# Kernel tuning notes

Measured on AMD Instinct MI355X. Metric: run time of the kernel, lower is better.

Reference implementation:

```python
import jax, jax.numpy as jnp
import numpy as np

K = 3  # kernel_size from init_kwargs


def setup_inputs() -> dict:
    key = jax.random.key(0)
    x = jax.random.normal(key, (32, 64, 56, 56), dtype=jnp.float32)
    return {"x": x}


def reference(x):
    # Faithful translation of Shift.forward: for each channel i, for each
    # (dy, dx) in the kernel window, emit the padded slice
    # x_pad[:, i, dy:dy+h, dx:dx+w]. Concatenation order is channel-major,
    # then row-major over (dy, dx), which equals stacking the k*k shifts on
    # a new axis right after the channel axis and flattening.
    n, c, h, w = x.shape
    pad = K // 2
    xp = jnp.pad(x, ((0, 0), (0, 0), (pad, pad), (pad, pad)))
    # k*k shifted views of shape [n, c, h, w]; loop is over a small fixed
    # offset set (9 for k=3), not over data dims.
    shifts = jnp.stack(
        [xp[:, :, dy:dy + h, dx:dx + w] for dy in range(K) for dx in range(K)],
        axis=2,
    )  # [n, c, k*k, h, w]
    return shifts.reshape(n, c * K * K, h, w)
```

## Files before the change

### kernel.cpp

```cpp
#include <hip/hip_runtime.h>


#define N_ 32
#define C_ 64
#define H_ 56
#define W_ 56
#define KK 9
#define W4 (W_ / 4)
#define ROW_F4 W4
#define OUT_F4 (N_ * C_ * KK * H_ * W4)

__global__ __launch_bounds__(256) void shift_kernel(const float* __restrict__ x,
                                                    float4* __restrict__ out) {
    int idx = blockIdx.x * blockDim.x + threadIdx.x;
    if (idx >= OUT_F4) return;

    int w4 = idx % W4;
    int t  = idx / W4;
    int h  = t % H_;
    t /= H_;
    int s  = t % KK;
    t /= KK;
    int c  = t % C_;
    int n  = t / C_;

    int dy = s / 3 - 1;
    int dx = s % 3 - 1;

    int ih = h + dy;

    float4 v;
    if (ih < 0 || ih >= H_) {
        v = make_float4(0.f, 0.f, 0.f, 0.f);
    } else {
        const float* row = x + (((long)(n * C_ + c) * H_) + ih) * W_;
        int w0 = w4 * 4 + dx;
        if (w4 > 0 && w4 < W4 - 1) {
            v.x = row[w0];
            v.y = row[w0 + 1];
            v.z = row[w0 + 2];
            v.w = row[w0 + 3];
        } else {
            int w1 = w0 + 1, w2 = w0 + 2, w3 = w0 + 3;
            v.x = (w0 >= 0 && w0 < W_) ? row[w0] : 0.f;
            v.y = (w1 >= 0 && w1 < W_) ? row[w1] : 0.f;
            v.z = (w2 >= 0 && w2 < W_) ? row[w2] : 0.f;
            v.w = (w3 >= 0 && w3 < W_) ? row[w3] : 0.f;
        }
    }
    out[idx] = v;
}

extern "C" void kernel_launch(void* const* d_in, const int* in_sizes, int n_in,
                              void* d_out, int out_size, void* d_ws, size_t ws_size,
                              hipStream_t stream) {
    const float* x = (const float*)d_in[0];
    float4* out = (float4*)d_out;

    int total = OUT_F4;
    int block = 256;
    int grid = (total + block - 1) / block;
    shift_kernel<<<grid, block, 0, stream>>>(x, out);
}
```

Measured before the change: 289.5 us.

## Compute all nine shifts per thread from three loaded rows with nontemporal stores

Each thread now handles one input position and loads its three neighbouring rows once (a float4 plus two halo scalars each). From those registers it emits all nine shifted outputs, instead of each thread reading input separately for every shift. Output writes use nontemporal float4 stores to avoid polluting the cache. This cuts redundant input reads and index math, but launches nine times fewer threads, each with more work and register use.

New measurement: 242.9 us. -16.1%, faster.

```diff
diff --git a/kernel.cpp b/kernel.cpp
--- a/kernel.cpp
+++ b/kernel.cpp
@@ -5,60 +5,65 @@
 #define C_ 64
 #define H_ 56
 #define W_ 56
-#define KK 9
-#define W4 (W_ / 4)
-#define ROW_F4 W4
-#define OUT_F4 (N_ * C_ * KK * H_ * W4)
+#define W4 14
+#define PLANE (H_ * W_)
+#define POS_PER_PLANE (H_ * W4)
+#define TOTAL (N_ * C_ * POS_PER_PLANE)
+
+typedef float f4 __attribute__((ext_vector_type(4)));
 
 __global__ __launch_bounds__(256) void shift_kernel(const float* __restrict__ x,
-                                                    float4* __restrict__ out) {
-    int idx = blockIdx.x * blockDim.x + threadIdx.x;
-    if (idx >= OUT_F4) return;
+                                                    float* __restrict__ out) {
+    int t = blockIdx.x * blockDim.x + threadIdx.x;
+    if (t >= TOTAL) return;
 
-    int w4 = idx % W4;
-    int t  = idx / W4;
-    int h  = t % H_;
-    t /= H_;
-    int s  = t % KK;
-    t /= KK;
-    int c  = t % C_;
-    int n  = t / C_;
+    int w4 = t % W4;
+    int r  = t / W4;
+    int h  = r % H_;
+    int nc = r / H_;
 
-    int dy = s / 3 - 1;
-    int dx = s % 3 - 1;
+    int w0 = w4 * 4;
+    const float* plane = x + (long)nc * PLANE;
 
-    int ih = h + dy;
-
-    float4 v;
-    if (ih < 0 || ih >= H_) {
-        v = make_float4(0.f, 0.f, 0.f, 0.f);
-    } else {
-        const float* row = x + (((long)(n * C_ + c) * H_) + ih) * W_;
-        int w0 = w4 * 4 + dx;
-        if (w4 > 0 && w4 < W4 - 1) {
-            v.x = row[w0];
-            v.y = row[w0 + 1];
-            v.z = row[w0 + 2];
-            v.w = row[w0 + 3];
+    float rowbuf[3][6];
+#pragma unroll
+    for (int d = 0; d < 3; ++d) {
+        int ih = h + d - 1;
+        if (ih < 0 || ih >= H_) {
+#pragma unroll
+            for (int j = 0; j < 6; ++j) rowbuf[d][j] = 0.f;
         } else {
-            int w1 = w0 + 1, w2 = w0 + 2, w3 = w0 + 3;
-            v.x = (w0 >= 0 && w0 < W_) ? row[w0] : 0.f;
-            v.y = (w1 >= 0 && w1 < W_) ? row[w1] : 0.f;
-            v.z = (w2 >= 0 && w2 < W_) ? row[w2] : 0.f;
-            v.w = (w3 >= 0 && w3 < W_) ? row[w3] : 0.f;
+            const float* rp = plane + ih * W_;
+            f4 v = *(const f4*)(rp + w0);
+            rowbuf[d][1] = v.x;
+            rowbuf[d][2] = v.y;
+            rowbuf[d][3] = v.z;
+            rowbuf[d][4] = v.w;
+            rowbuf[d][0] = (w4 > 0)      ? rp[w0 - 1] : 0.f;
+            rowbuf[d][5] = (w4 < W4 - 1) ? rp[w0 + 4] : 0.f;
         }
     }
-    out[idx] = v;
+
+    float* ob = out + ((long)(nc * 9) * H_ + h) * W_ + w0;
+#pragma unroll
+    for (int dy = 0; dy < 3; ++dy) {
+#pragma unroll
+        for (int dx = 0; dx < 3; ++dx) {
+            f4 v = { rowbuf[dy][dx],     rowbuf[dy][dx + 1],
+                     rowbuf[dy][dx + 2], rowbuf[dy][dx + 3] };
+            f4* dst = (f4*)(ob + (long)(dy * 3 + dx) * PLANE);
+            __builtin_nontemporal_store(v, dst);
+        }
+    }
 }
 
 extern "C" void kernel_launch(void* const* d_in, const int* in_sizes, int n_in,
                               void* d_out, int out_size, void* d_ws, size_t ws_size,
                               hipStream_t stream) {
     const float* x = (const float*)d_in[0];
-    float4* out = (float4*)d_out;
+    float* out = (float*)d_out;
 
-    int total = OUT_F4;
     int block = 256;
-    int grid = (total + block - 1) / block;
+    int grid = (TOTAL + block - 1) / block;
     shift_kernel<<<grid, block, 0, stream>>>(x, out);
 }
```
